# Performance work log

Measured on AMD Instinct MI355X. Metric: run time of the kernel, lower is better.

## Reference

```python
import jax, jax.numpy as jnp
import numpy as np

B, C, H, W = 4, 64, 64, 64
CQ = C // 8

def setup_inputs() -> dict:
    key = jax.random.key(0)
    ks = jax.random.split(key, 8)
    s = 1.0 / np.sqrt(C)
    return {
        "x": jax.random.normal(ks[0], (B, C, H, W), dtype=jnp.float32),
        "Wq": jax.random.normal(ks[1], (CQ, C), dtype=jnp.float32) * s,
        "bq": jax.random.normal(ks[2], (CQ,), dtype=jnp.float32) * 0.01,
        "Wk": jax.random.normal(ks[3], (CQ, C), dtype=jnp.float32) * s,
        "bk": jax.random.normal(ks[4], (CQ,), dtype=jnp.float32) * 0.01,
        "Wv": jax.random.normal(ks[5], (C, C), dtype=jnp.float32) * s,
        "bv": jax.random.normal(ks[6], (C,), dtype=jnp.float32) * 0.01,
        "gamma": jax.random.normal(ks[7], (1,), dtype=jnp.float32) * 0.1,
    }

def reference(x, Wq, bq, Wk, bk, Wv, bv, gamma):
    b, c, h, w = x.shape
    n = h * w
    xf = x.reshape(b, c, n)  # [B, C, N]
    # 1x1 convs are pointwise channel projections
    q = jnp.einsum('oc,bcn->bon', Wq, xf) + bq[None, :, None]  # [B, CQ, N]
    k = jnp.einsum('oc,bcn->bon', Wk, xf) + bk[None, :, None]  # [B, CQ, N]
    v = jnp.einsum('oc,bcn->bon', Wv, xf) + bv[None, :, None]  # [B, C, N]
    energy = jnp.einsum('bcn,bcm->bnm', q, k)                  # [B, N, N]
    attn = jax.nn.softmax(energy, axis=-1)
    out = jnp.einsum('bcm,bnm->bcn', v, attn)                  # [B, C, N]
    out = out.reshape(b, c, h, w)
    return gamma[0] * out + x
```

## Files before the change

### kernel.cpp

```cpp
#include <hip/hip_runtime.h>
#include <hip/hip_bf16.h>


typedef __attribute__((ext_vector_type(8))) short short8;
typedef __attribute__((ext_vector_type(4))) float f32x4;
typedef unsigned short ushort_t;

#define NSEQ 4096
#define LOG2E 1.4426950408889634f

__device__ __forceinline__ unsigned pk_bf16(float lo, float hi) {
  union { __hip_bfloat16 b; unsigned short u; } cl, ch;
  cl.b = __float2bfloat16(lo);
  ch.b = __float2bfloat16(hi);
  return (unsigned)cl.u | ((unsigned)ch.u << 16);
}

__global__ __launch_bounds__(256) void proj_kernel(
    const float* __restrict__ x,
    const float* __restrict__ Wq, const float* __restrict__ bq,
    const float* __restrict__ Wk, const float* __restrict__ bk,
    const float* __restrict__ Wv, const float* __restrict__ bv,
    ushort_t* __restrict__ Qb, ushort_t* __restrict__ Kb,
    ushort_t* __restrict__ Vb)
{
  const int tid  = threadIdx.x;
  const int lane = tid & 63;
  const int w    = __builtin_amdgcn_readfirstlane(tid >> 6);
  const int blk  = blockIdx.x;
  const int b    = blk >> 6;
  const int n    = (blk & 63) * 64 + lane;

  const float* xb = x + (size_t)(b * 64) * NSEQ + n;

  const int cv0 = w * 16;
  float av[16];
#pragma unroll
  for (int j = 0; j < 16; ++j) av[j] = bv[cv0 + j];

  const bool isq = (w < 2);
  const int qkb  = (w & 1) * 4;
  const float* Wr = isq ? Wq : Wk;
  const float* br = isq ? bq : bk;
  float aqk[4];
#pragma unroll
  for (int j = 0; j < 4; ++j) aqk[j] = br[qkb + j];

#pragma unroll
  for (int kc = 0; kc < 64; kc += 8) {
    float xv[8];
#pragma unroll
    for (int i = 0; i < 8; ++i) xv[i] = xb[(size_t)(kc + i) * NSEQ];
#pragma unroll
    for (int i = 0; i < 8; ++i) {
      const float xk = xv[i];
#pragma unroll
      for (int j = 0; j < 16; ++j) av[j] += Wv[(cv0 + j) * 64 + kc + i] * xk;
#pragma unroll
      for (int j = 0; j < 4; ++j) aqk[j] += Wr[(qkb + j) * 64 + kc + i] * xk;
    }
  }

  union { __hip_bfloat16 h; ushort_t u; } cv;
  ushort_t* vt = Vb + ((size_t)(b * 128 + (n >> 5)) * 64 + cv0) * 32 + (n & 31);
#pragma unroll
  for (int j = 0; j < 16; ++j) {
    cv.h = __float2bfloat16(av[j]);
    vt[j * 32] = cv.u;
  }

  if (isq) {
#pragma unroll
    for (int j = 0; j < 4; ++j) aqk[j] *= LOG2E;
  }
  union { unsigned u[2]; ulong1 l; } pkd;
  pkd.u[0] = pk_bf16(aqk[0], aqk[1]);
  pkd.u[1] = pk_bf16(aqk[2], aqk[3]);
  ushort_t* qk = (isq ? Qb : Kb) + ((size_t)(b * NSEQ + n)) * 8 + qkb;
  *(ulong1*)qk = pkd.l;
}

__global__ __launch_bounds__(512, 4) void attn_kernel(
    const ushort_t* __restrict__ Qb, const ushort_t* __restrict__ Kb,
    const ushort_t* __restrict__ Vb, const float* __restrict__ x,
    const float* __restrict__ gamma, float* __restrict__ out)
{
  __shared__ float buf[4][64][36];

  const int tid  = threadIdx.x;
  const int wave = __builtin_amdgcn_readfirstlane(tid >> 6);
  const int lane = tid & 63;
  const int q16  = lane & 15;
  const int quad = lane >> 4;
  const int blk  = blockIdx.x;
  const int b    = blk >> 7;
  const int n0   = (blk & 127) << 5;
  const int mbase = wave << 9;

  const short8 z8 = {0, 0, 0, 0, 0, 0, 0, 0};
  short8 qfA = *(const short8*)(Qb + ((size_t)(b * NSEQ + n0 + q16)) * 8);
  short8 qfB = *(const short8*)(Qb + ((size_t)(b * NSEQ + n0 + 16 + q16)) * 8);
  if (quad != 0) { qfA = z8; qfB = z8; }

  const int mperm = 8 * (q16 >> 2) + (q16 & 3);
  const char* kbase = (const char*)(Kb + ((size_t)(b * NSEQ + mbase + mperm)) * 8);
  const char* vbase = (const char*)(Vb + ((size_t)(b * 128 + (mbase >> 5)) * 64) * 32);
  const int voff = q16 * 64 + quad * 16;

  f32x4 aA0 = {0.f, 0.f, 0.f, 0.f};
  f32x4 aA1 = aA0, aA2 = aA0, aA3 = aA0;
  f32x4 aB0 = aA0, aB1 = aA0, aB2 = aA0, aB3 = aA0;
  float lA = 0.f, lB = 0.f;

  short8 kf0 = *(const short8*)(kbase);
  short8 kf1 = *(const short8*)(kbase + 64);
  short8 vf0 = *(const short8*)(vbase + voff);
  short8 vf1 = *(const short8*)(vbase + voff + 1024);
  short8 vf2 = *(const short8*)(vbase + voff + 2048);
  short8 vf3 = *(const short8*)(vbase + voff + 3072);

#pragma unroll 2
  for (int t = 0; t < 16; ++t) {
    const int tn = (t + 1 < 16) ? (t + 1) : 15;
    const size_t ko = (size_t)tn * 512;
    const size_t vo = (size_t)tn * 4096 + voff;
    short8 nk0 = *(const short8*)(kbase + ko);
    short8 nk1 = *(const short8*)(kbase + ko + 64);
    short8 nv0 = *(const short8*)(vbase + vo);
    short8 nv1 = *(const short8*)(vbase + vo + 1024);
    short8 nv2 = *(const short8*)(vbase + vo + 2048);
    short8 nv3 = *(const short8*)(vbase + vo + 3072);

    const f32x4 z = {0.f, 0.f, 0.f, 0.f};
    f32x4 s0 = __builtin_amdgcn_mfma_f32_16x16x32_bf16(kf0, qfA, z, 0, 0, 0);
    f32x4 s1 = __builtin_amdgcn_mfma_f32_16x16x32_bf16(kf1, qfA, z, 0, 0, 0);
    f32x4 s2 = __builtin_amdgcn_mfma_f32_16x16x32_bf16(kf0, qfB, z, 0, 0, 0);
    f32x4 s3 = __builtin_amdgcn_mfma_f32_16x16x32_bf16(kf1, qfB, z, 0, 0, 0);

    float pA0 = __builtin_amdgcn_exp2f(s0[0]);
    float pA1 = __builtin_amdgcn_exp2f(s0[1]);
    float pA2 = __builtin_amdgcn_exp2f(s0[2]);
    float pA3 = __builtin_amdgcn_exp2f(s0[3]);
    float pA4 = __builtin_amdgcn_exp2f(s1[0]);
    float pA5 = __builtin_amdgcn_exp2f(s1[1]);
    float pA6 = __builtin_amdgcn_exp2f(s1[2]);
    float pA7 = __builtin_amdgcn_exp2f(s1[3]);
    float pB0 = __builtin_amdgcn_exp2f(s2[0]);
    float pB1 = __builtin_amdgcn_exp2f(s2[1]);
    float pB2 = __builtin_amdgcn_exp2f(s2[2]);
    float pB3 = __builtin_amdgcn_exp2f(s2[3]);
    float pB4 = __builtin_amdgcn_exp2f(s3[0]);
    float pB5 = __builtin_amdgcn_exp2f(s3[1]);
    float pB6 = __builtin_amdgcn_exp2f(s3[2]);
    float pB7 = __builtin_amdgcn_exp2f(s3[3]);
    lA += ((pA0 + pA1) + (pA2 + pA3)) + ((pA4 + pA5) + (pA6 + pA7));
    lB += ((pB0 + pB1) + (pB2 + pB3)) + ((pB4 + pB5) + (pB6 + pB7));

    union { unsigned u[4]; short8 s; } uA, uB;
    uA.u[0] = pk_bf16(pA0, pA1); uA.u[1] = pk_bf16(pA2, pA3);
    uA.u[2] = pk_bf16(pA4, pA5); uA.u[3] = pk_bf16(pA6, pA7);
    uB.u[0] = pk_bf16(pB0, pB1); uB.u[1] = pk_bf16(pB2, pB3);
    uB.u[2] = pk_bf16(pB4, pB5); uB.u[3] = pk_bf16(pB6, pB7);
    const short8 pfA = uA.s;
    const short8 pfB = uB.s;

    aA0 = __builtin_amdgcn_mfma_f32_16x16x32_bf16(vf0, pfA, aA0, 0, 0, 0);
    aA1 = __builtin_amdgcn_mfma_f32_16x16x32_bf16(vf1, pfA, aA1, 0, 0, 0);
    aA2 = __builtin_amdgcn_mfma_f32_16x16x32_bf16(vf2, pfA, aA2, 0, 0, 0);
    aA3 = __builtin_amdgcn_mfma_f32_16x16x32_bf16(vf3, pfA, aA3, 0, 0, 0);
    aB0 = __builtin_amdgcn_mfma_f32_16x16x32_bf16(vf0, pfB, aB0, 0, 0, 0);
    aB1 = __builtin_amdgcn_mfma_f32_16x16x32_bf16(vf1, pfB, aB1, 0, 0, 0);
    aB2 = __builtin_amdgcn_mfma_f32_16x16x32_bf16(vf2, pfB, aB2, 0, 0, 0);
    aB3 = __builtin_amdgcn_mfma_f32_16x16x32_bf16(vf3, pfB, aB3, 0, 0, 0);

    kf0 = nk0; kf1 = nk1;
    vf0 = nv0; vf1 = nv1; vf2 = nv2; vf3 = nv3;
  }

  lA += __shfl_xor(lA, 16); lA += __shfl_xor(lA, 32);
  lB += __shfl_xor(lB, 16); lB += __shfl_xor(lB, 32);

  f32x4 aAs[4] = {aA0, aA1, aA2, aA3};
  f32x4 aBs[4] = {aB0, aB1, aB2, aB3};

  if (wave >= 4) {
    float* d = &buf[wave - 4][lane][0];
#pragma unroll
    for (int j = 0; j < 4; ++j)
#pragma unroll
      for (int r = 0; r < 4; ++r) {
        d[j * 4 + r]      = aAs[j][r];
        d[16 + j * 4 + r] = aBs[j][r];
      }
    d[32] = lA; d[33] = lB;
  }
  __syncthreads();
  if (wave < 4) {
    float* d = &buf[wave][lane][0];
#pragma unroll
    for (int j = 0; j < 4; ++j)
#pragma unroll
      for (int r = 0; r < 4; ++r) {
        aAs[j][r] += d[j * 4 + r];
        aBs[j][r] += d[16 + j * 4 + r];
      }
    lA += d[32]; lB += d[33];
#pragma unroll
    for (int j = 0; j < 4; ++j)
#pragma unroll
      for (int r = 0; r < 4; ++r) {
        d[j * 4 + r]      = aAs[j][r];
        d[16 + j * 4 + r] = aBs[j][r];
      }
    d[32] = lA; d[33] = lB;
  }
  __syncthreads();

  const int qt = wave >> 2;
  const int cg = wave & 3;
  float fr[4] = {0.f, 0.f, 0.f, 0.f};
  float lt = 0.f;
#pragma unroll
  for (int w2 = 0; w2 < 4; ++w2) {
    lt += buf[w2][lane][32 + qt];
#pragma unroll
    for (int r = 0; r < 4; ++r) fr[r] += buf[w2][lane][qt * 16 + cg * 4 + r];
  }

  const float g = gamma[0];
  const float ginv = g / lt;
  const int nn = n0 + qt * 16 + q16;
#pragma unroll
  for (int r = 0; r < 4; ++r) {
    const int c = cg * 16 + quad * 4 + r;
    const size_t idx = ((size_t)(b * 64 + c)) * NSEQ + nn;
    out[idx] = fr[r] * ginv + x[idx];
  }
}

extern "C" void kernel_launch(void* const* d_in, const int* in_sizes, int n_in,
                              void* d_out, int out_size, void* d_ws, size_t ws_size,
                              hipStream_t stream) {
  (void)in_sizes; (void)n_in; (void)out_size; (void)ws_size;
  const float* x     = (const float*)d_in[0];
  const float* Wq    = (const float*)d_in[1];
  const float* bq    = (const float*)d_in[2];
  const float* Wk    = (const float*)d_in[3];
  const float* bk    = (const float*)d_in[4];
  const float* Wv    = (const float*)d_in[5];
  const float* bv    = (const float*)d_in[6];
  const float* gamma = (const float*)d_in[7];
  float* out = (float*)d_out;

  ushort_t* Qb = (ushort_t*)d_ws;
  ushort_t* Kb = (ushort_t*)((char*)d_ws + (256u << 10));
  ushort_t* Vb = (ushort_t*)((char*)d_ws + (512u << 10));

  hipLaunchKernelGGL(proj_kernel, dim3(256), dim3(256), 0, stream,
                     x, Wq, bq, Wk, bk, Wv, bv, Qb, Kb, Vb);
  hipLaunchKernelGGL(attn_kernel, dim3(512), dim3(512), 0, stream,
                     Qb, Kb, Vb, x, gamma, out);
}
```

Baseline: 111.0 us.

## Split projection across 4x more blocks and drop manual K/V register prefetch

The projection kernel now launches four times as many blocks. Each wave computes 4 V channels plus one Q/K channel instead of 16 V channels plus four Q/K channels, which raises parallelism and lowers register pressure. The trade-off is that each block rereads x, and Q/K are written as scalar bf16 stores. In the attention loop, the explicit next-iteration register prefetch of K/V fragments is removed and loads are issued directly per iteration, leaving latency hiding to the compiler and occupancy. The remaining edits are cosmetic rewrites of the bf16 packing using bit_cast.

```diff
diff --git a/kernel.cpp b/kernel.cpp
--- a/kernel.cpp
+++ b/kernel.cpp
@@ -4,19 +4,19 @@
 
 typedef __attribute__((ext_vector_type(8))) short short8;
 typedef __attribute__((ext_vector_type(4))) float f32x4;
+typedef __attribute__((ext_vector_type(4))) unsigned uint4v;
 typedef unsigned short ushort_t;
 
 #define NSEQ 4096
 #define LOG2E 1.4426950408889634f
 
 __device__ __forceinline__ unsigned pk_bf16(float lo, float hi) {
-  union { __hip_bfloat16 b; unsigned short u; } cl, ch;
-  cl.b = __float2bfloat16(lo);
-  ch.b = __float2bfloat16(hi);
-  return (unsigned)cl.u | ((unsigned)ch.u << 16);
-}
-
-__global__ __launch_bounds__(256) void proj_kernel(
+  const unsigned short a = __builtin_bit_cast(unsigned short, __float2bfloat16(lo));
+  const unsigned short b = __builtin_bit_cast(unsigned short, __float2bfloat16(hi));
+  return (unsigned)a | ((unsigned)b << 16);
+}
+
+__global__ __launch_bounds__(256, 4) void proj_kernel(
     const float* __restrict__ x,
     const float* __restrict__ Wq, const float* __restrict__ bq,
     const float* __restrict__ Wk, const float* __restrict__ bk,
@@ -28,23 +28,21 @@
   const int lane = tid & 63;
   const int w    = __builtin_amdgcn_readfirstlane(tid >> 6);
   const int blk  = blockIdx.x;
-  const int b    = blk >> 6;
-  const int n    = (blk & 63) * 64 + lane;
+  const int quarter = blk & 3;
+  const int g    = (blk >> 2) & 63;
+  const int b    = blk >> 8;
+  const int n    = g * 64 + lane;
 
   const float* xb = x + (size_t)(b * 64) * NSEQ + n;
-
-  const int cv0 = w * 16;
-  float av[16];
-#pragma unroll
-  for (int j = 0; j < 16; ++j) av[j] = bv[cv0 + j];
-
-  const bool isq = (w < 2);
-  const int qkb  = (w & 1) * 4;
-  const float* Wr = isq ? Wq : Wk;
-  const float* br = isq ? bq : bk;
-  float aqk[4];
-#pragma unroll
-  for (int j = 0; j < 4; ++j) aqk[j] = br[qkb + j];
+  const int co0 = quarter * 16 + w * 4;
+  const float* w0 = Wv + (co0 + 0) * 64;
+  const float* w1 = Wv + (co0 + 1) * 64;
+  const float* w2 = Wv + (co0 + 2) * 64;
+  const float* w3 = Wv + (co0 + 3) * 64;
+  const int p = quarter * 4 + w;
+  const float* wr = (p < 8) ? (Wq + p * 64) : (Wk + (p - 8) * 64);
+  float a0 = bv[co0 + 0], a1 = bv[co0 + 1], a2 = bv[co0 + 2], a3 = bv[co0 + 3];
+  float aq = (p < 8) ? bq[p] : bk[p - 8];
 
 #pragma unroll
   for (int kc = 0; kc < 64; kc += 8) {
@@ -54,30 +52,23 @@
 #pragma unroll
     for (int i = 0; i < 8; ++i) {
       const float xk = xv[i];
-#pragma unroll
-      for (int j = 0; j < 16; ++j) av[j] += Wv[(cv0 + j) * 64 + kc + i] * xk;
-#pragma unroll
-      for (int j = 0; j < 4; ++j) aqk[j] += Wr[(qkb + j) * 64 + kc + i] * xk;
+      a0 += w0[kc + i] * xk;
+      a1 += w1[kc + i] * xk;
+      a2 += w2[kc + i] * xk;
+      a3 += w3[kc + i] * xk;
+      aq += wr[kc + i] * xk;
     }
   }
 
-  union { __hip_bfloat16 h; ushort_t u; } cv;
-  ushort_t* vt = Vb + ((size_t)(b * 128 + (n >> 5)) * 64 + cv0) * 32 + (n & 31);
-#pragma unroll
-  for (int j = 0; j < 16; ++j) {
-    cv.h = __float2bfloat16(av[j]);
-    vt[j * 32] = cv.u;
-  }
-
-  if (isq) {
-#pragma unroll
-    for (int j = 0; j < 4; ++j) aqk[j] *= LOG2E;
-  }
-  union { unsigned u[2]; ulong1 l; } pkd;
-  pkd.u[0] = pk_bf16(aqk[0], aqk[1]);
-  pkd.u[1] = pk_bf16(aqk[2], aqk[3]);
-  ushort_t* qk = (isq ? Qb : Kb) + ((size_t)(b * NSEQ + n)) * 8 + qkb;
-  *(ulong1*)qk = pkd.l;
+  ushort_t* vt = Vb + ((size_t)(b * 128 + (n >> 5)) * 64 + co0) * 32 + (n & 31);
+  vt[0]  = __builtin_bit_cast(ushort_t, __float2bfloat16(a0));
+  vt[32] = __builtin_bit_cast(ushort_t, __float2bfloat16(a1));
+  vt[64] = __builtin_bit_cast(ushort_t, __float2bfloat16(a2));
+  vt[96] = __builtin_bit_cast(ushort_t, __float2bfloat16(a3));
+
+  if (p < 8) aq *= LOG2E;
+  ushort_t* qk = ((p < 8) ? Qb : Kb) + ((size_t)(b * NSEQ + n)) * 8 + (p & 7);
+  *qk = __builtin_bit_cast(ushort_t, __float2bfloat16(aq));
 }
 
 __global__ __launch_bounds__(512, 4) void attn_kernel(
@@ -104,32 +95,24 @@
 
   const int mperm = 8 * (q16 >> 2) + (q16 & 3);
   const char* kbase = (const char*)(Kb + ((size_t)(b * NSEQ + mbase + mperm)) * 8);
-  const char* vbase = (const char*)(Vb + ((size_t)(b * 128 + (mbase >> 5)) * 64) * 32);
-  const int voff = q16 * 64 + quad * 16;
+  const char* vbase = (const char*)(Vb + ((size_t)(b * 128 + (mbase >> 5)) * 64) * 32)
+                      + q16 * 64 + quad * 16;
 
   f32x4 aA0 = {0.f, 0.f, 0.f, 0.f};
   f32x4 aA1 = aA0, aA2 = aA0, aA3 = aA0;
   f32x4 aB0 = aA0, aB1 = aA0, aB2 = aA0, aB3 = aA0;
   float lA = 0.f, lB = 0.f;
 
-  short8 kf0 = *(const short8*)(kbase);
-  short8 kf1 = *(const short8*)(kbase + 64);
-  short8 vf0 = *(const short8*)(vbase + voff);
-  short8 vf1 = *(const short8*)(vbase + voff + 1024);
-  short8 vf2 = *(const short8*)(vbase + voff + 2048);
-  short8 vf3 = *(const short8*)(vbase + voff + 3072);
-
 #pragma unroll 2
   for (int t = 0; t < 16; ++t) {
-    const int tn = (t + 1 < 16) ? (t + 1) : 15;
-    const size_t ko = (size_t)tn * 512;
-    const size_t vo = (size_t)tn * 4096 + voff;
-    short8 nk0 = *(const short8*)(kbase + ko);
-    short8 nk1 = *(const short8*)(kbase + ko + 64);
-    short8 nv0 = *(const short8*)(vbase + vo);
-    short8 nv1 = *(const short8*)(vbase + vo + 1024);
-    short8 nv2 = *(const short8*)(vbase + vo + 2048);
-    short8 nv3 = *(const short8*)(vbase + vo + 3072);
+    const char* kp = kbase + (size_t)t * 512;
+    const char* vp = vbase + (size_t)t * 4096;
+    const short8 kf0 = *(const short8*)(kp);
+    const short8 kf1 = *(const short8*)(kp + 64);
+    const short8 vf0 = *(const short8*)(vp);
+    const short8 vf1 = *(const short8*)(vp + 1024);
+    const short8 vf2 = *(const short8*)(vp + 2048);
+    const short8 vf3 = *(const short8*)(vp + 3072);
 
     const f32x4 z = {0.f, 0.f, 0.f, 0.f};
     f32x4 s0 = __builtin_amdgcn_mfma_f32_16x16x32_bf16(kf0, qfA, z, 0, 0, 0);
@@ -156,13 +139,12 @@
     lA += ((pA0 + pA1) + (pA2 + pA3)) + ((pA4 + pA5) + (pA6 + pA7));
     lB += ((pB0 + pB1) + (pB2 + pB3)) + ((pB4 + pB5) + (pB6 + pB7));
 
-    union { unsigned u[4]; short8 s; } uA, uB;
-    uA.u[0] = pk_bf16(pA0, pA1); uA.u[1] = pk_bf16(pA2, pA3);
-    uA.u[2] = pk_bf16(pA4, pA5); uA.u[3] = pk_bf16(pA6, pA7);
-    uB.u[0] = pk_bf16(pB0, pB1); uB.u[1] = pk_bf16(pB2, pB3);
-    uB.u[2] = pk_bf16(pB4, pB5); uB.u[3] = pk_bf16(pB6, pB7);
-    const short8 pfA = uA.s;
-    const short8 pfB = uB.s;
+    const uint4v uA = {pk_bf16(pA0, pA1), pk_bf16(pA2, pA3),
+                       pk_bf16(pA4, pA5), pk_bf16(pA6, pA7)};
+    const uint4v uB = {pk_bf16(pB0, pB1), pk_bf16(pB2, pB3),
+                       pk_bf16(pB4, pB5), pk_bf16(pB6, pB7)};
+    const short8 pfA = __builtin_bit_cast(short8, uA);
+    const short8 pfB = __builtin_bit_cast(short8, uB);
 
     aA0 = __builtin_amdgcn_mfma_f32_16x16x32_bf16(vf0, pfA, aA0, 0, 0, 0);
     aA1 = __builtin_amdgcn_mfma_f32_16x16x32_bf16(vf1, pfA, aA1, 0, 0, 0);
@@ -172,9 +154,6 @@
     aB1 = __builtin_amdgcn_mfma_f32_16x16x32_bf16(vf1, pfB, aB1, 0, 0, 0);
     aB2 = __builtin_amdgcn_mfma_f32_16x16x32_bf16(vf2, pfB, aB2, 0, 0, 0);
     aB3 = __builtin_amdgcn_mfma_f32_16x16x32_bf16(vf3, pfB, aB3, 0, 0, 0);
-
-    kf0 = nk0; kf1 = nk1;
-    vf0 = nv0; vf1 = nv1; vf2 = nv2; vf3 = nv3;
   }
 
   lA += __shfl_xor(lA, 16); lA += __shfl_xor(lA, 32);
@@ -227,8 +206,7 @@
     for (int r = 0; r < 4; ++r) fr[r] += buf[w2][lane][qt * 16 + cg * 4 + r];
   }
 
-  const float g = gamma[0];
-  const float ginv = g / lt;
+  const float ginv = gamma[0] / lt;
   const int nn = n0 + qt * 16 + q16;
 #pragma unroll
   for (int r = 0; r < 4; ++r) {
@@ -256,7 +234,7 @@
   ushort_t* Kb = (ushort_t*)((char*)d_ws + (256u << 10));
   ushort_t* Vb = (ushort_t*)((char*)d_ws + (512u << 10));
 
-  hipLaunchKernelGGL(proj_kernel, dim3(256), dim3(256), 0, stream,
+  hipLaunchKernelGGL(proj_kernel, dim3(1024), dim3(256), 0, stream,
                      x, Wq, bq, Wk, bk, Wv, bv, Qb, Kb, Vb);
   hipLaunchKernelGGL(attn_kernel, dim3(512), dim3(512), 0, stream,
                      Qb, Kb, Vb, x, gamma, out);
```

Result: faster. 96.10 us (-13.4%).
